# Optimization experiments

Measured on AMD Instinct MI355X. Metric: run time of the kernel, lower is better.

## Reference

```python
import jax, jax.numpy as jnp
import numpy as np

COST_CLASS = 1.0
COST_BBOX = 1.0
COST_GIOU = 1.0
COST_MASK_CE = 1.0
COST_MASK_DICE = 1.0
ALPHA = 0.25   # hardcoded in forward (focal alpha)
GAMMA = 2.0


def box_cxcywh_to_xyxy(b):
    cx, cy, w, h = jnp.split(b, 4, axis=-1)
    return jnp.concatenate([cx - 0.5 * w, cy - 0.5 * h, cx + 0.5 * w, cy + 0.5 * h], axis=-1)


def generalized_box_iou(b1, b2):
    # b1 [N,4], b2 [M,4] in xyxy -> [N,M]
    a1 = (b1[:, 2] - b1[:, 0]) * (b1[:, 3] - b1[:, 1])
    a2 = (b2[:, 2] - b2[:, 0]) * (b2[:, 3] - b2[:, 1])
    lt = jnp.maximum(b1[:, None, :2], b2[None, :, :2])
    rb = jnp.minimum(b1[:, None, 2:], b2[None, :, 2:])
    wh = jnp.clip(rb - lt, 0.0)
    inter = wh[..., 0] * wh[..., 1]
    union = a1[:, None] + a2[None, :] - inter
    iou = inter / union
    ltc = jnp.minimum(b1[:, None, :2], b2[None, :, :2])
    rbc = jnp.maximum(b1[:, None, 2:], b2[None, :, 2:])
    whc = jnp.clip(rbc - ltc, 0.0)
    area = whc[..., 0] * whc[..., 1]
    return iou - (area - union) / area


def point_sample_bilinear(masks, coords):
    # masks [N,H,W], coords [P,2] in [0,1] (x,y); grid_sample align_corners=False,
    # zero padding: pixel = coord*size - 0.5. Fully batched over N and P.
    H, W = masks.shape[-2:]
    x = coords[:, 0] * W - 0.5
    y = coords[:, 1] * H - 0.5
    x0 = jnp.floor(x); y0 = jnp.floor(y)
    wx = x - x0; wy = y - y0
    x0i = x0.astype(jnp.int32); y0i = y0.astype(jnp.int32)
    def g(yi, xi):
        valid = ((xi >= 0) & (xi < W) & (yi >= 0) & (yi < H)).astype(masks.dtype)
        v = masks[:, jnp.clip(yi, 0, H - 1), jnp.clip(xi, 0, W - 1)]  # [N,P]
        return v * valid
    return (g(y0i, x0i) * (1 - wy) * (1 - wx) + g(y0i, x0i + 1) * (1 - wy) * wx
            + g(y0i + 1, x0i) * wy * (1 - wx) + g(y0i + 1, x0i + 1) * wy * wx)


def point_sample_nearest(masks, coords):
    H, W = masks.shape[-2:]
    xi = jnp.round(coords[:, 0] * W - 0.5).astype(jnp.int32)
    yi = jnp.round(coords[:, 1] * H - 0.5).astype(jnp.int32)
    valid = ((xi >= 0) & (xi < W) & (yi >= 0) & (yi < H)).astype(masks.dtype)
    return masks[:, jnp.clip(yi, 0, H - 1), jnp.clip(xi, 0, W - 1)] * valid


def _cost_single(logits, boxes, labels, tboxes, pmasks, tmasks, pts):
    # logits [Q,C], boxes [Q,4], labels [T], tboxes [T,4],
    # pmasks [Q,H,W], tmasks [T,H,W] (0/1 int), pts [P,2]
    prob = jax.nn.sigmoid(logits)
    neg_cost = (1 - ALPHA) * prob ** GAMMA * (-jax.nn.log_sigmoid(-logits))
    pos_cost = ALPHA * (1 - prob) ** GAMMA * (-jax.nn.log_sigmoid(logits))
    cost_class = jnp.take(pos_cost, labels, axis=1) - jnp.take(neg_cost, labels, axis=1)  # [Q,T]
    giou = generalized_box_iou(box_cxcywh_to_xyxy(boxes), box_cxcywh_to_xyxy(tboxes))
    cost_bbox = jnp.abs(boxes[:, None, :] - tboxes[None, :, :]).sum(-1)  # L1 cdist
    C = COST_BBOX * cost_bbox + COST_CLASS * cost_class - COST_GIOU * giou
    # batched point sampling (replaces per-query / per-target python loops)
    pm = point_sample_bilinear(pmasks, pts)                    # [Q,P]
    tm = point_sample_nearest(tmasks.astype(pmasks.dtype), pts)  # [T,P]
    P = pm.shape[-1]
    # batch_sigmoid_ce_loss: pairwise BCE-with-logits, mean over points
    pos_ce = jax.nn.softplus(-pm)  # loss if target==1
    neg_ce = jax.nn.softplus(pm)   # loss if target==0
    ce = (pos_ce @ tm.T + neg_ce @ (1.0 - tm).T) / P
    # batch_dice_loss
    sm = jax.nn.sigmoid(pm)
    num = 2.0 * (sm @ tm.T)
    den = sm.sum(-1)[:, None] + tm.sum(-1)[None, :]
    dice = 1.0 - (num + 1.0) / (den + 1.0)
    C = C + COST_MASK_CE * ce + COST_MASK_DICE * dice
    # replicate C[C.isinf()|C.isnan()] = 2*max
    finite = jnp.isfinite(C)
    mx = jnp.max(jnp.where(finite, C, -jnp.inf))
    return jnp.where(finite, C, 2.0 * mx)


def setup_inputs() -> dict:
    key = jax.random.key(0)
    ks = jax.random.split(key, 7)
    bs, Q, C, T, H, W = 2, 900, 91, 100, 128, 128
    P = H * W // 16  # mask_point_sample_ratio = 16
    return {
        "pred_logits": jax.random.normal(ks[0], (bs, Q, C), jnp.float32),
        "pred_boxes": jax.random.uniform(ks[1], (bs, Q, 4), jnp.float32),
        "tgt_labels": jax.random.randint(ks[2], (bs, T), 0, C, jnp.int32),
        "tgt_boxes": jax.random.uniform(ks[3], (bs, T, 4), jnp.float32),
        "pred_masks": jax.random.normal(ks[4], (bs, Q, H, W), jnp.float32),
        "tgt_masks": jax.random.randint(ks[5], (bs, T, H, W), 0, 2, jnp.int32),
        "point_coords": jax.random.uniform(ks[6], (bs, P, 2), jnp.float32),
    }


def reference(pred_logits, pred_boxes, tgt_labels, tgt_boxes, pred_masks, tgt_masks, point_coords):
    # Returns the per-image matching cost matrices [bs, Q, T]; the CPU-side
    # Hungarian solve (scipy linear_sum_assignment) consumes these.
    return jax.vmap(_cost_single)(pred_logits, pred_boxes, tgt_labels, tgt_boxes,
                                  pred_masks, tgt_masks, point_coords)
```

## Files before the change

### kernel.cpp

```cpp
#include <hip/hip_runtime.h>
#include <math.h>

#define QN 900
#define TN 100
#define CN 91
#define PN 1024
#define HWD 128
#define BS 2

typedef float f32x2 __attribute__((ext_vector_type(2)));

__device__ __forceinline__ float sigmoidf_(float x) {
    return 1.0f / (1.0f + __expf(-x));
}
__device__ __forceinline__ float softplusf_(float x) {
    return fmaxf(x, 0.0f) + __logf(1.0f + __expf(-fabsf(x)));
}
__device__ __forceinline__ unsigned bfhi(float f) {
    unsigned u = __float_as_uint(f);
    return (u + 0x7FFFu + ((u >> 16) & 1u)) & 0xFFFF0000u;
}

__global__ __launch_bounds__(1024) void sort_kernel(
    const float2* __restrict__ coords, uint4* __restrict__ table)
{
    __shared__ unsigned key[PN];
    const int b = blockIdx.x;
    const int tid = threadIdx.x;

    {
        float2 cd = coords[b * PN + tid];
        float x = cd.x * (float)HWD - 0.5f;
        float y = cd.y * (float)HWD - 0.5f;
        int x0 = (int)floorf(x);
        int y0 = (int)floorf(y);
        int xl = min(max(x0, 0), HWD - 2);
        int yc0 = min(max(y0, 0), HWD - 1);
        unsigned ar0 = (unsigned)(yc0 * HWD + xl);
        key[tid] = (ar0 << 10) | (unsigned)tid;
    }
    for (int k = 2; k <= PN; k <<= 1) {
        for (int j = k >> 1; j > 0; j >>= 1) {
            __syncthreads();
            int ixj = tid ^ j;
            if (ixj > tid) {
                unsigned a = key[tid], c = key[ixj];
                bool up = ((tid & k) == 0);
                if ((a > c) == up) { key[tid] = c; key[ixj] = a; }
            }
        }
    }
    __syncthreads();

    const int idx = (int)(key[tid] & 1023u);
    float2 cd = coords[b * PN + idx];
    float x = cd.x * (float)HWD - 0.5f;
    float y = cd.y * (float)HWD - 0.5f;
    float fx = floorf(x), fy = floorf(y);
    int x0 = (int)fx, y0 = (int)fy;
    int y1 = y0 + 1;
    float wx = x - fx, wy = y - fy;
    bool bx0, bx1;
    int xl;
    if (x0 < 0)            { xl = 0;       bx0 = true;  bx1 = false; wx = 1.f - wx; }
    else if (x0 >= HWD-1)  { xl = HWD - 2; bx0 = false; bx1 = true;  wx = 1.f - wx; }
    else                   { xl = x0;      bx0 = true;  bx1 = true; }
    bool by0 = (y0 >= 0) & (y0 < HWD);
    bool by1 = (y1 >= 0) & (y1 < HWD);
    int yc0 = min(max(y0, 0), HWD - 1), yc1 = min(max(y1, 0), HWD - 1);
    unsigned ar0 = (unsigned)(yc0 * HWD + xl);
    unsigned ar1 = (unsigned)(yc1 * HWD + xl);
    unsigned fl = (unsigned)bx0 | ((unsigned)bx1 << 1) |
                  ((unsigned)by0 << 2) | ((unsigned)by1 << 3);
    int xi = (int)rintf(cd.x * (float)HWD - 0.5f);
    int yi = (int)rintf(cd.y * (float)HWD - 0.5f);
    unsigned nvalid = (xi >= 0) & (xi < HWD) & (yi >= 0) & (yi < HWD);
    unsigned naddr = (unsigned)(min(max(yi, 0), HWD - 1) * HWD + min(max(xi, 0), HWD - 1));

    uint4 te;
    te.x = ar0 | (ar1 << 14) | (fl << 28);
    te.y = __float_as_uint(wx);
    te.z = __float_as_uint(wy);
    te.w = naddr | (nvalid << 14);
    table[b * PN + tid] = te;
}

__global__ __launch_bounds__(256) void prep_kernel(
    const uint4* __restrict__ table, const int* __restrict__ tmasks,
    unsigned* __restrict__ tmw, float* __restrict__ tmsum)
{
    __shared__ int cnt[4];
    const int bx = blockIdx.x;
    const int tid = threadIdx.x;
    const int wv = tid >> 6, lane = tid & 63;
    const int b = bx / TN, t = bx % TN;
    const int* m = tmasks + (size_t)(b * TN + t) * (HWD * HWD);
    int addr[4]; unsigned vld[4];
#pragma unroll
    for (int c = 0; c < 4; ++c) {
        unsigned w = table[b * PN + c * 256 + tid].w;
        addr[c] = (int)(w & 16383u);
        vld[c] = w >> 14;
    }
    int rv[4];
#pragma unroll
    for (int c = 0; c < 4; ++c) rv[c] = m[addr[c]];
    int mycnt = 0;
#pragma unroll
    for (int c = 0; c < 4; ++c) {
        unsigned long long bal = __ballot(vld[c] && (rv[c] != 0));
        if (lane == 0) {
            tmw[(size_t)(b * TN + t) * 32 + c * 8 + wv * 2 + 0] = (unsigned)(bal & 0xFFFFFFFFull);
            tmw[(size_t)(b * TN + t) * 32 + c * 8 + wv * 2 + 1] = (unsigned)(bal >> 32);
            mycnt += __popcll(bal);
        }
    }
    if (lane == 0) cnt[wv] = mycnt;
    __syncthreads();
    if (tid == 0)
        tmsum[b * TN + t] = (float)((cnt[0] + cnt[1]) + (cnt[2] + cnt[3]));
}

__global__ __launch_bounds__(256, 4) void main_kernel(
    const float* __restrict__ logits, const float4* __restrict__ pboxes,
    const int* __restrict__ labels, const float4* __restrict__ tboxes,
    const float* __restrict__ pmasks, const uint4* __restrict__ table,
    const unsigned* __restrict__ tmw, const float* __restrict__ tmsum_,
    float* __restrict__ out, float* __restrict__ blockmax,
    int* __restrict__ badflag)
{
    __shared__ unsigned pl[PN];
    __shared__ float part[8][32][9];
    __shared__ float sred[8];
    __shared__ float mred[256];
    __shared__ int sbad;

    const int bq = blockIdx.x;
    const int b = bq / QN, q = bq - b * QN;
    const int tid = threadIdx.x;
    const int wv = tid >> 6, lane = tid & 63;
    const int pc = tid >> 5, ts = tid & 31;
    const float* mask = pmasks + (size_t)bq * (HWD * HWD);

    if (tid == 0) sbad = 0;

    unsigned fl[4];
    float wxa[4], wya[4];
    int ar0[4], ar1[4];
#pragma unroll
    for (int c = 0; c < 4; ++c) {
        uint4 te = table[b * PN + c * 256 + tid];
        ar0[c] = (int)(te.x & 16383u);
        ar1[c] = (int)((te.x >> 14) & 16383u);
        fl[c] = te.x >> 28;
        wxa[c] = __uint_as_float(te.y);
        wya[c] = __uint_as_float(te.z);
    }

    f32x2 p0[4], p1[4];
#pragma unroll
    for (int c = 0; c < 4; ++c) {
        p0[c] = *(const f32x2*)(mask + ar0[c]);
        p1[c] = *(const f32x2*)(mask + ar1[c]);
    }

    const unsigned* rowb = tmw + (size_t)b * TN * 32;
    unsigned w0[4], w1[4], w2[4], w3[4];
#pragma unroll
    for (int g = 0; g < 4; ++g) {
        w0[g] = rowb[(ts +  0) * 32 + pc * 4 + g];
        w1[g] = rowb[(ts + 32) * 32 + pc * 4 + g];
        w2[g] = rowb[(ts + 64) * 32 + pc * 4 + g];
        w3[g] = (ts + 96 < TN) ? rowb[(ts + 96) * 32 + pc * 4 + g] : 0u;
    }
    float lg = 0.f, tsum = 0.f;
    float4 tb = make_float4(0, 0, 0, 0), pb = make_float4(0, 0, 0, 0);
    if (tid < TN) {
        int lab = labels[b * TN + tid];
        lg = logits[(size_t)(b * QN + q) * CN + lab];
        tsum = tmsum_[b * TN + tid];
        tb = tboxes[b * TN + tid];
        pb = pboxes[b * QN + q];
    }

    float lsp = 0.f, lsm = 0.f;
#pragma unroll
    for (int c = 0; c < 4; ++c) {
        const bool bx0 = fl[c] & 1u, bx1 = fl[c] & 2u, by0 = fl[c] & 4u, by1 = fl[c] & 8u;
        float v00 = (by0 && bx0) ? p0[c].x : 0.f;
        float v01 = (by0 && bx1) ? p0[c].y : 0.f;
        float v10 = (by1 && bx0) ? p1[c].x : 0.f;
        float v11 = (by1 && bx1) ? p1[c].y : 0.f;
        float wx = wxa[c], wy = wya[c];
        float pm = (v00 * (1.f - wx) + v01 * wx) * (1.f - wy) +
                   (v10 * (1.f - wx) + v11 * wx) * wy;
        float sg = sigmoidf_(pm);
        lsp += softplusf_(pm);
        lsm += sg;
        pl[c * 256 + tid] = bfhi(pm) | (bfhi(sg) >> 16);
    }
    for (int off = 32; off > 0; off >>= 1) {
        lsp += __shfl_down(lsp, off);
        lsm += __shfl_down(lsm, off);
    }
    if (lane == 0) { sred[wv * 2 + 0] = lsp; sred[wv * 2 + 1] = lsm; }
    __syncthreads();
    float s_sp = (sred[0] + sred[2]) + (sred[4] + sred[6]);
    float s_sm = (sred[1] + sred[3]) + (sred[5] + sred[7]);

    float a0 = 0, a1 = 0, a2 = 0, a3 = 0, a4 = 0, a5 = 0, a6 = 0, a7 = 0;
#pragma unroll
    for (int g = 0; g < 4; ++g) {
        unsigned u0 = w0[g], u1 = w1[g], u2 = w2[g], u3 = w3[g];
        int p0i = pc * 128 + g * 32;
#pragma unroll
        for (int jj = 0; jj < 8; ++jj) {
            uint4 u = *(const uint4*)&pl[p0i + jj * 4];
#pragma unroll
            for (int k = 0; k < 4; ++k) {
                unsigned uv = (k == 0) ? u.x : (k == 1) ? u.y : (k == 2) ? u.z : u.w;
                float pmv = __uint_as_float(uv & 0xFFFF0000u);
                float sgv = __uint_as_float(uv << 16);
                float f0 = (float)((u0 >> k) & 1u);
                float f1 = (float)((u1 >> k) & 1u);
                float f2 = (float)((u2 >> k) & 1u);
                float f3 = (float)((u3 >> k) & 1u);
                a0 = fmaf(pmv, f0, a0); a1 = fmaf(sgv, f0, a1);
                a2 = fmaf(pmv, f1, a2); a3 = fmaf(sgv, f1, a3);
                a4 = fmaf(pmv, f2, a4); a5 = fmaf(sgv, f2, a5);
                a6 = fmaf(pmv, f3, a6); a7 = fmaf(sgv, f3, a7);
            }
            u0 >>= 4; u1 >>= 4; u2 >>= 4; u3 >>= 4;
        }
    }
    part[pc][ts][0] = a0; part[pc][ts][1] = a1;
    part[pc][ts][2] = a2; part[pc][ts][3] = a3;
    part[pc][ts][4] = a4; part[pc][ts][5] = a5;
    part[pc][ts][6] = a6; part[pc][ts][7] = a7;
    __syncthreads();

    float val = -INFINITY;
    if (tid < TN) {
        int t = tid, tss = t & 31, kk = t >> 5;
        float apm = 0.f, asg = 0.f;
#pragma unroll
        for (int pp = 0; pp < 8; ++pp) {
            apm += part[pp][tss][kk * 2 + 0];
            asg += part[pp][tss][kk * 2 + 1];
        }
        float ce = (s_sp - apm) * (1.0f / (float)PN);
        float dice = 1.0f - (2.0f * asg + 1.0f) / (s_sm + tsum + 1.0f);

        float pr = sigmoidf_(lg);
        float cls = 0.25f * (1.f - pr) * (1.f - pr) * softplusf_(-lg)
                  - 0.75f * pr * pr * softplusf_(lg);

        float l1 = fabsf(pb.x - tb.x) + fabsf(pb.y - tb.y) +
                   fabsf(pb.z - tb.z) + fabsf(pb.w - tb.w);

        float px1 = pb.x - 0.5f * pb.z, py1 = pb.y - 0.5f * pb.w;
        float px2 = pb.x + 0.5f * pb.z, py2 = pb.y + 0.5f * pb.w;
        float tx1 = tb.x - 0.5f * tb.z, ty1 = tb.y - 0.5f * tb.w;
        float tx2 = tb.x + 0.5f * tb.z, ty2 = tb.y + 0.5f * tb.w;
        float A1 = (px2 - px1) * (py2 - py1);
        float A2 = (tx2 - tx1) * (ty2 - ty1);
        float iw = fmaxf(fminf(px2, tx2) - fmaxf(px1, tx1), 0.f);
        float ih = fmaxf(fminf(py2, ty2) - fmaxf(py1, ty1), 0.f);
        float inter = iw * ih;
        float uni = A1 + A2 - inter;
        float iou = inter / uni;
        float cw = fmaxf(fmaxf(px2, tx2) - fminf(px1, tx1), 0.f);
        float chh = fmaxf(fmaxf(py2, ty2) - fminf(py1, ty1), 0.f);
        float area = cw * chh;
        float giou = iou - (area - uni) / area;

        float Cv = l1 + cls - giou + ce + dice;
        out[(size_t)(b * QN + q) * TN + t] = Cv;
        if (isfinite(Cv)) val = Cv;
        else sbad = 1;
    }
    mred[tid] = val;
    __syncthreads();
    if (tid < 64) {
        float m = fmaxf(fmaxf(mred[tid], mred[tid + 64]),
                        fmaxf(mred[tid + 128], mred[tid + 192]));
        for (int off = 32; off > 0; off >>= 1)
            m = fmaxf(m, __shfl_down(m, off));
        if (tid == 0) { blockmax[bq] = m; badflag[bq] = sbad; }
    }
}

__global__ __launch_bounds__(128) void fix_kernel(float* __restrict__ out,
                                                  const float* __restrict__ blockmax,
                                                  const int* __restrict__ badflag)
{
    const int bq = blockIdx.x;
    if (badflag[bq] == 0) return;
    const int tid = threadIdx.x;
    if (tid >= TN) return;
    const int b = bq / QN;
    float v = out[(size_t)bq * TN + tid];
    if (!isfinite(v)) {
        float m = -INFINITY;
        for (int k = 0; k < QN; ++k) m = fmaxf(m, blockmax[b * QN + k]);
        out[(size_t)bq * TN + tid] = 2.0f * m;
    }
}

extern "C" void kernel_launch(void* const* d_in, const int* in_sizes, int n_in,
                              void* d_out, int out_size, void* d_ws, size_t ws_size,
                              hipStream_t stream) {
    const float* logits  = (const float*)d_in[0];
    const float4* pboxes = (const float4*)d_in[1];
    const int* labels    = (const int*)d_in[2];
    const float4* tboxes = (const float4*)d_in[3];
    const float* pmasks  = (const float*)d_in[4];
    const int* tmasks    = (const int*)d_in[5];
    const float* coords  = (const float*)d_in[6];
    float* out = (float*)d_out;

    char* ws = (char*)d_ws;
    unsigned* tmw   = (unsigned*)(ws);
    float* tmsum    = (float*)(ws + 25600);
    float* blockmax = (float*)(ws + 26400);
    int* badflag    = (int*)(ws + 33600);
    uint4* table    = (uint4*)(ws + 40960);

    hipLaunchKernelGGL(sort_kernel, dim3(BS), dim3(1024), 0, stream,
                       (const float2*)coords, table);
    hipLaunchKernelGGL(prep_kernel, dim3(BS * TN), dim3(256), 0, stream,
                       table, tmasks, tmw, tmsum);
    hipLaunchKernelGGL(main_kernel, dim3(BS * QN), dim3(256), 0, stream,
                       logits, pboxes, labels, tboxes, pmasks, table,
                       tmw, tmsum, out, blockmax, badflag);
    hipLaunchKernelGGL(fix_kernel, dim3(BS * QN), dim3(128), 0, stream,
                       out, blockmax, badflag);
}
```

Baseline: 55.90 us.

## Replace bitonic sort of sample points with row-bucketed counting sort

The bitonic sort over 1024 point keys, which needed about 55 barrier-separated passes, is replaced by a stable counting sort keyed only on the clamped row. Ranks within a wavefront come from shuffles, and per-wave histograms go through shared atomics and prefix sums. The goal is cheaper preprocessing for the ordering of the point table. Points are now ordered by row only, not by row then column, which may slightly change gather locality in later kernels.

```diff
diff --git a/kernel.cpp b/kernel.cpp
--- a/kernel.cpp
+++ b/kernel.cpp
@@ -24,50 +24,67 @@
 __global__ __launch_bounds__(1024) void sort_kernel(
     const float2* __restrict__ coords, uint4* __restrict__ table)
 {
-    __shared__ unsigned key[PN];
+    __shared__ int whist[16][HWD];
+    __shared__ int woff[16][HWD];
+    __shared__ int rowtot[HWD];
+    __shared__ int rowbase[HWD];
+    __shared__ unsigned short perm[PN];
+
     const int b = blockIdx.x;
     const int tid = threadIdx.x;
-
-    {
-        float2 cd = coords[b * PN + tid];
-        float x = cd.x * (float)HWD - 0.5f;
-        float y = cd.y * (float)HWD - 0.5f;
-        int x0 = (int)floorf(x);
-        int y0 = (int)floorf(y);
-        int xl = min(max(x0, 0), HWD - 2);
-        int yc0 = min(max(y0, 0), HWD - 1);
-        unsigned ar0 = (unsigned)(yc0 * HWD + xl);
-        key[tid] = (ar0 << 10) | (unsigned)tid;
-    }
-    for (int k = 2; k <= PN; k <<= 1) {
-        for (int j = k >> 1; j > 0; j >>= 1) {
-            __syncthreads();
-            int ixj = tid ^ j;
-            if (ixj > tid) {
-                unsigned a = key[tid], c = key[ixj];
-                bool up = ((tid & k) == 0);
-                if ((a > c) == up) { key[tid] = c; key[ixj] = a; }
-            }
-        }
-    }
-    __syncthreads();
-
-    const int idx = (int)(key[tid] & 1023u);
-    float2 cd = coords[b * PN + idx];
+    const int wv = tid >> 6, lane = tid & 63;
+
+    ((int*)whist)[tid] = 0;
+    ((int*)whist)[tid + 1024] = 0;
+    __syncthreads();
+
+    float2 cd = coords[b * PN + tid];
+    float yf = cd.y * (float)HWD - 0.5f;
+    int y0 = (int)floorf(yf);
+    const int r = min(max(y0, 0), HWD - 1);
+
+    int rank = 0;
+    for (int j = 0; j < 64; ++j) {
+        int rj = __shfl(r, j);
+        rank += (j < lane) & (rj == r);
+    }
+    atomicAdd(&whist[wv][r], 1);
+    __syncthreads();
+
+    if (tid < HWD) {
+        int acc = 0;
+#pragma unroll
+        for (int w = 0; w < 16; ++w) { woff[w][tid] = acc; acc += whist[w][tid]; }
+        rowtot[tid] = acc;
+    }
+    __syncthreads();
+    if (tid == 0) {
+        int acc = 0;
+        for (int rr = 0; rr < HWD; ++rr) { rowbase[rr] = acc; acc += rowtot[rr]; }
+    }
+    __syncthreads();
+
+    const int slot = rowbase[r] + woff[wv][r] + rank;
+    perm[slot] = (unsigned short)tid;
+    __syncthreads();
+
+    const int idx = (int)perm[tid];
+    cd = coords[b * PN + idx];
     float x = cd.x * (float)HWD - 0.5f;
     float y = cd.y * (float)HWD - 0.5f;
     float fx = floorf(x), fy = floorf(y);
-    int x0 = (int)fx, y0 = (int)fy;
-    int y1 = y0 + 1;
+    int x0 = (int)fx;
+    int py0 = (int)fy;
+    int py1 = py0 + 1;
     float wx = x - fx, wy = y - fy;
     bool bx0, bx1;
     int xl;
-    if (x0 < 0)            { xl = 0;       bx0 = true;  bx1 = false; wx = 1.f - wx; }
-    else if (x0 >= HWD-1)  { xl = HWD - 2; bx0 = false; bx1 = true;  wx = 1.f - wx; }
-    else                   { xl = x0;      bx0 = true;  bx1 = true; }
-    bool by0 = (y0 >= 0) & (y0 < HWD);
-    bool by1 = (y1 >= 0) & (y1 < HWD);
-    int yc0 = min(max(y0, 0), HWD - 1), yc1 = min(max(y1, 0), HWD - 1);
+    if (x0 < 0)             { xl = 0;       bx0 = true;  bx1 = false; wx = 1.f - wx; }
+    else if (x0 >= HWD - 1) { xl = HWD - 2; bx0 = false; bx1 = true;  wx = 1.f - wx; }
+    else                    { xl = x0;      bx0 = true;  bx1 = true; }
+    bool by0 = (py0 >= 0) & (py0 < HWD);
+    bool by1 = (py1 >= 0) & (py1 < HWD);
+    int yc0 = min(max(py0, 0), HWD - 1), yc1 = min(max(py1, 0), HWD - 1);
     unsigned ar0 = (unsigned)(yc0 * HWD + xl);
     unsigned ar1 = (unsigned)(yc1 * HWD + xl);
     unsigned fl = (unsigned)bx0 | ((unsigned)bx1 << 1) |
```

Result: faster. 53.40 us (-4.5%).
